# Kernel tuning notes

Hardware: AMD Instinct MI355X
Metric: run time of the kernel (lower is better)

Reference implementation:

```python
import jax, jax.numpy as jnp
import numpy as np

N_NODES = 50000
N_EDGES = 800000
IN_DIM, HID_DIM, OUT_DIM = 128, 128, 64


def _sage_conv(x, src, dst, W_l, W_r, b, num_nodes):
    # mean aggregation of source-node features onto destination nodes
    msg = x[src]  # [E, d] gather
    summed = jax.ops.segment_sum(msg, dst, num_segments=num_nodes)  # [N, d]
    deg = jax.ops.segment_sum(jnp.ones((src.shape[0],), dtype=x.dtype), dst,
                              num_segments=num_nodes)  # [N]
    agg = summed / jnp.maximum(deg, 1.0)[:, None]
    # SAGEConv: lin_l(agg) + lin_r(x); bias only on lin_l (PyG default)
    return agg @ W_l + b + x @ W_r


def setup_inputs() -> dict:
    key = jax.random.key(0)
    k = jax.random.split(key, 8)
    def glorot(kk, shape):
        lim = float(np.sqrt(6.0 / (shape[0] + shape[1])))
        return jax.random.uniform(kk, shape, jnp.float32, -lim, lim)
    return {
        "x": jax.random.normal(k[0], (N_NODES, IN_DIM), jnp.float32),
        "edge_index": jax.random.randint(k[1], (2, N_EDGES), 0, N_NODES, jnp.int64),
        "W1_l": glorot(k[2], (IN_DIM, HID_DIM)),
        "W1_r": glorot(k[3], (IN_DIM, HID_DIM)),
        "b1": jnp.zeros((HID_DIM,), jnp.float32),
        "W2_l": glorot(k[4], (HID_DIM, OUT_DIM)),
        "W2_r": glorot(k[5], (HID_DIM, OUT_DIM)),
        "b2": jnp.zeros((OUT_DIM,), jnp.float32),
    }


def reference(x, edge_index, W1_l, W1_r, b1, W2_l, W2_r, b2):
    src, dst = edge_index[0], edge_index[1]
    n = x.shape[0]
    h = _sage_conv(x, src, dst, W1_l, W1_r, b1, n)
    h = jax.nn.relu(h)
    # dropout is identity in eval mode
    out = _sage_conv(h, src, dst, W2_l, W2_r, b2, n)
    return out
```

## Files before the change

### kernel.cpp

```cpp
#include <hip/hip_runtime.h>
#include <hip/hip_bf16.h>


#define BLK 256

typedef __attribute__((ext_vector_type(8))) short short8;
typedef __attribute__((ext_vector_type(4))) float f32x4;

__device__ inline unsigned short f2bf(float f) {
    unsigned int u = __builtin_bit_cast(unsigned int, f);
    u += 0x7fffu + ((u >> 16) & 1u);
    return (unsigned short)(u >> 16);
}
__device__ inline float bf2f(unsigned short h) {
    return __builtin_bit_cast(float, ((unsigned int)h) << 16);
}


__global__ __launch_bounds__(BLK) void deg_count_kernel(const int* __restrict__ dst,
                                                        int E, int* __restrict__ deg) {
    int e = blockIdx.x * BLK + threadIdx.x;
    if (e < E) atomicAdd(&deg[dst[e]], 1);
}

__global__ __launch_bounds__(BLK) void partial_sum_kernel(const int* __restrict__ deg,
                                                          int n, int* __restrict__ partials) {
    __shared__ int s[BLK];
    int t = threadIdx.x;
    int idx = blockIdx.x * BLK + t;
    s[t] = (idx < n) ? deg[idx] : 0;
    __syncthreads();
    for (int o = BLK / 2; o > 0; o >>= 1) {
        if (t < o) s[t] += s[t + o];
        __syncthreads();
    }
    if (t == 0) partials[blockIdx.x] = s[0];
}

__global__ __launch_bounds__(BLK) void scan_partials_kernel(int* __restrict__ partials, int n) {
    __shared__ int s[BLK];
    int t = threadIdx.x;
    int v = (t < n) ? partials[t] : 0;
    s[t] = v;
    __syncthreads();
    int sum = v;
    for (int o = 1; o < BLK; o <<= 1) {
        int other = (t >= o) ? s[t - o] : 0;
        __syncthreads();
        sum += other;
        s[t] = sum;
        __syncthreads();
    }
    if (t < n) partials[t] = sum - v;
}

__global__ __launch_bounds__(BLK) void chunk_scan_kernel(const int* __restrict__ deg,
                                                         const int* __restrict__ partials,
                                                         int n, int* __restrict__ row_start) {
    __shared__ int s[BLK];
    int t = threadIdx.x;
    int idx = blockIdx.x * BLK + t;
    int v = (idx < n) ? deg[idx] : 0;
    s[t] = v;
    __syncthreads();
    int sum = v;
    for (int o = 1; o < BLK; o <<= 1) {
        int other = (t >= o) ? s[t - o] : 0;
        __syncthreads();
        sum += other;
        s[t] = sum;
        __syncthreads();
    }
    if (idx < n) row_start[idx] = (sum - v) + partials[blockIdx.x];
}

__global__ __launch_bounds__(BLK) void fill_kernel(const int* __restrict__ src,
                                                   const int* __restrict__ dst, int E,
                                                   const int* __restrict__ row_start,
                                                   int* __restrict__ cursor,
                                                   int* __restrict__ csr_src) {
    int e = blockIdx.x * BLK + threadIdx.x;
    if (e >= E) return;
    int d = dst[e];
    int pos = atomicAdd(&cursor[d], 1);
    atomicExch(&csr_src[row_start[d] + pos], src[e]);
}


__global__ __launch_bounds__(BLK) void f32_to_bf16_kernel(const float* __restrict__ in,
                                                          unsigned short* __restrict__ out,
                                                          int nquad) {
    int i = blockIdx.x * BLK + threadIdx.x;
    if (i >= nquad) return;
    float4 v = ((const float4*)in)[i];
    ushort4 o;
    o.x = f2bf(v.x); o.y = f2bf(v.y); o.z = f2bf(v.z); o.w = f2bf(v.w);
    ((ushort4*)out)[i] = o;
}

__global__ __launch_bounds__(BLK) void pack_all_w_kernel(const float* __restrict__ W1l,
                                                         const float* __restrict__ W1r,
                                                         const float* __restrict__ W2l,
                                                         const float* __restrict__ W2r,
                                                         unsigned short* __restrict__ P1l,
                                                         unsigned short* __restrict__ P1r,
                                                         unsigned short* __restrict__ P2l,
                                                         unsigned short* __restrict__ P2r) {
    int t = blockIdx.x * BLK + threadIdx.x;
    const float* W;
    unsigned short* P;
    int Ncol, local;
    if (t < 16384)      { W = W1l; P = P1l; Ncol = 128; local = t; }
    else if (t < 32768) { W = W1r; P = P1r; Ncol = 128; local = t - 16384; }
    else if (t < 40960) { W = W2l; P = P2l; Ncol = 64;  local = t - 32768; }
    else if (t < 49152) { W = W2r; P = P2r; Ncol = 64;  local = t - 40960; }
    else return;
    int j = local & 7;
    int lane = (local >> 3) & 63;
    int rest = local >> 9;
    int nt = Ncol >> 4;
    int n16 = rest % nt, kb = rest / nt;
    int k = kb * 32 + (lane >> 4) * 8 + j;
    int c = n16 * 16 + (lane & 15);
    P[local] = f2bf(W[(size_t)k * Ncol + c]);
}


__global__ __launch_bounds__(BLK) void agg_bf16_kernel(const unsigned short* __restrict__ feat,
                                                       const int* __restrict__ row_start,
                                                       const int* __restrict__ deg,
                                                       const int* __restrict__ csr_src,
                                                       unsigned short* __restrict__ out,
                                                       int n_nodes) {
    int gid = blockIdx.x * (BLK / 64) + (threadIdx.x >> 6);
    int lane = threadIdx.x & 63;
    if (gid >= n_nodes) return;
    int start = row_start[gid];
    int cnt = deg[gid];
    const unsigned int* fp = (const unsigned int*)feat;
    float ax[8], ay[8];
#pragma unroll
    for (int j = 0; j < 8; j++) { ax[j] = 0.f; ay[j] = 0.f; }

    for (int base = 0; base < cnt; base += 64) {
        int rem = cnt - base;
        int m = rem < 64 ? rem : 64;
        int idx = csr_src[start + base + (lane < m ? lane : m - 1)];
        int e = 0;
        for (; e + 8 <= m; e += 8) {
            unsigned int v[8];
#pragma unroll
            for (int j = 0; j < 8; j++) {
                int s = __shfl(idx, e + j);
                v[j] = fp[(size_t)s * 64 + lane];
            }
#pragma unroll
            for (int j = 0; j < 8; j++) {
                ax[j] += bf2f((unsigned short)v[j]);
                ay[j] += bf2f((unsigned short)(v[j] >> 16));
            }
        }
        for (; e < m; ++e) {
            int s = __shfl(idx, e);
            unsigned int v = fp[(size_t)s * 64 + lane];
            ax[0] += bf2f((unsigned short)v);
            ay[0] += bf2f((unsigned short)(v >> 16));
        }
    }
    float sx = ((ax[0] + ax[1]) + (ax[2] + ax[3])) + ((ax[4] + ax[5]) + (ax[6] + ax[7]));
    float sy = ((ay[0] + ay[1]) + (ay[2] + ay[3])) + ((ay[4] + ay[5]) + (ay[6] + ay[7]));
    float inv = 1.0f / fmaxf((float)cnt, 1.0f);
    unsigned int packed = (unsigned int)f2bf(sx * inv) | ((unsigned int)f2bf(sy * inv) << 16);
    ((unsigned int*)out)[(size_t)gid * 64 + lane] = packed;
}


template <int NCOL, bool RELU, bool OUT_BF16>
__global__ __launch_bounds__(BLK) void gemm_mfma_kernel(const unsigned short* __restrict__ A1,
                                                        const unsigned short* __restrict__ A2,
                                                        const unsigned short* __restrict__ Pl,
                                                        const unsigned short* __restrict__ Pr,
                                                        const float* __restrict__ bias,
                                                        void* __restrict__ outp, int M) {
    constexpr int NT = NCOL / 16;
    const int wave = threadIdx.x >> 6, lane = threadIdx.x & 63;
    const int r0 = blockIdx.x * 128 + wave * 32;
    const int arow = lane & 15, kgrp = lane >> 4;

    f32x4 acc[2][NT];
#pragma unroll
    for (int h = 0; h < 2; h++)
#pragma unroll
        for (int n = 0; n < NT; n++) acc[h][n] = (f32x4){0.f, 0.f, 0.f, 0.f};

    const int ra = min(r0 + arow, M - 1);
    const int rb = min(r0 + 16 + arow, M - 1);

#pragma unroll
    for (int mat = 0; mat < 2; ++mat) {
        const unsigned short* A = mat ? A2 : A1;
        const unsigned short* P = mat ? Pr : Pl;
        const unsigned short* Aa = A + (size_t)ra * 128 + kgrp * 8;
        const unsigned short* Ab = A + (size_t)rb * 128 + kgrp * 8;
#pragma unroll
        for (int kb = 0; kb < 4; ++kb) {
            short8 afa = *(const short8*)(Aa + kb * 32);
            short8 afb = *(const short8*)(Ab + kb * 32);
            const unsigned short* Pk = P + (size_t)kb * NT * 512 + lane * 8;
#pragma unroll
            for (int n = 0; n < NT; ++n) {
                short8 wf = *(const short8*)(Pk + n * 512);
                acc[0][n] = __builtin_amdgcn_mfma_f32_16x16x32_bf16(afa, wf, acc[0][n], 0, 0, 0);
                acc[1][n] = __builtin_amdgcn_mfma_f32_16x16x32_bf16(afb, wf, acc[1][n], 0, 0, 0);
            }
        }
    }

#pragma unroll
    for (int n = 0; n < NT; ++n) {
        int col = n * 16 + arow;
        float bv = bias[col];
#pragma unroll
        for (int h = 0; h < 2; ++h) {
#pragma unroll
            for (int i = 0; i < 4; ++i) {
                int row = r0 + h * 16 + kgrp * 4 + i;
                if (row < M) {
                    float v = acc[h][n][i] + bv;
                    if (RELU) v = fmaxf(v, 0.f);
                    if (OUT_BF16)
                        ((unsigned short*)outp)[(size_t)row * NCOL + col] = f2bf(v);
                    else
                        ((float*)outp)[(size_t)row * NCOL + col] = v;
                }
            }
        }
    }
}


extern "C" void kernel_launch(void* const* d_in, const int* in_sizes, int n_in,
                              void* d_out, int out_size, void* d_ws, size_t ws_size,
                              hipStream_t stream) {
    const float* x   = (const float*)d_in[0];
    const int*   ei  = (const int*)d_in[1];
    const float* W1l = (const float*)d_in[2];
    const float* W1r = (const float*)d_in[3];
    const float* b1  = (const float*)d_in[4];
    const float* W2l = (const float*)d_in[5];
    const float* W2r = (const float*)d_in[6];
    const float* b2  = (const float*)d_in[7];
    float* out = (float*)d_out;

    const int N = in_sizes[0] / 128;
    const int E = in_sizes[1] / 2;
    const int* src = ei;
    const int* dst = ei + E;

    char* ws = (char*)d_ws;
    size_t off = 0;
    auto carve = [&](size_t bytes) {
        void* p = ws + off;
        off += (bytes + 255) & ~(size_t)255;
        return p;
    };
    int* deg       = (int*)carve((size_t)2 * N * 4);
    int* cursor    = deg + N;
    int* row_start = (int*)carve((size_t)N * 4);
    int* partials  = (int*)carve(256 * 4);
    int* csr_src   = (int*)carve((size_t)E * 4);
    unsigned short* xb   = (unsigned short*)carve((size_t)N * 128 * 2);
    unsigned short* aggb = (unsigned short*)carve((size_t)N * 128 * 2);
    unsigned short* hb   = (unsigned short*)carve((size_t)N * 128 * 2);
    unsigned short* P1l  = (unsigned short*)carve(128 * 128 * 2);
    unsigned short* P1r  = (unsigned short*)carve(128 * 128 * 2);
    unsigned short* P2l  = (unsigned short*)carve(128 * 64 * 2);
    unsigned short* P2r  = (unsigned short*)carve(128 * 64 * 2);

    hipMemsetAsync(deg, 0, (size_t)2 * N * 4, stream);

    const int nquad = N * 128 / 4;
    f32_to_bf16_kernel<<<(nquad + BLK - 1) / BLK, BLK, 0, stream>>>(x, xb, nquad);
    pack_all_w_kernel<<<192, BLK, 0, stream>>>(W1l, W1r, W2l, W2r, P1l, P1r, P2l, P2r);

    const int nchunk = (N + BLK - 1) / BLK;
    deg_count_kernel<<<(E + BLK - 1) / BLK, BLK, 0, stream>>>(dst, E, deg);
    partial_sum_kernel<<<nchunk, BLK, 0, stream>>>(deg, N, partials);
    scan_partials_kernel<<<1, BLK, 0, stream>>>(partials, nchunk);
    chunk_scan_kernel<<<nchunk, BLK, 0, stream>>>(deg, partials, N, row_start);
    fill_kernel<<<(E + BLK - 1) / BLK, BLK, 0, stream>>>(src, dst, E, row_start, cursor, csr_src);

    const int aggGrid = (N + 3) / 4;
    const int gemmGrid = (N + 127) / 128;

    agg_bf16_kernel<<<aggGrid, BLK, 0, stream>>>(xb, row_start, deg, csr_src, aggb, N);
    gemm_mfma_kernel<128, true, true><<<gemmGrid, BLK, 0, stream>>>(aggb, xb, P1l, P1r, b1, hb, N);
    agg_bf16_kernel<<<aggGrid, BLK, 0, stream>>>(hb, row_start, deg, csr_src, aggb, N);
    gemm_mfma_kernel<64, false, false><<<gemmGrid, BLK, 0, stream>>>(aggb, hb, P2l, P2r, b2, out, N);
}
```

Measured before the change: 303.8 us.

## Slice features into XCD-local column blocks and partition CSR fill by destination range

Stores bf16 node features in 8 column slices of 16 features each, so each slice (N*32 bytes, about 1.6 MB) can stay resident in one XCD's L2. Aggregation blocks are interleaved by slice using blockIdx&7, and each wave gathers 8 edges at a time with 8 lanes per edge, then reduces across lanes with shuffles. The CSR fill is split by destination range per blockIdx octet with plain stores instead of atomicExch, aiming for L2-local atomics. The trade-off is 8x redundant reads of dst in the fill and of the CSR indices in the gather, more shuffle reductions, and strided A-operand loads in the GEMM. It also relies on blockIdx-to-XCD round-robin placement.

```diff
diff --git a/kernel.cpp b/kernel.cpp
--- a/kernel.cpp
+++ b/kernel.cpp
@@ -74,29 +74,46 @@
     if (idx < n) row_start[idx] = (sum - v) + partials[blockIdx.x];
 }
 
-__global__ __launch_bounds__(BLK) void fill_kernel(const int* __restrict__ src,
-                                                   const int* __restrict__ dst, int E,
-                                                   const int* __restrict__ row_start,
-                                                   int* __restrict__ cursor,
-                                                   int* __restrict__ csr_src) {
-    int e = blockIdx.x * BLK + threadIdx.x;
-    if (e >= E) return;
-    int d = dst[e];
-    int pos = atomicAdd(&cursor[d], 1);
-    atomicExch(&csr_src[row_start[d] + pos], src[e]);
-}
-
-
-__global__ __launch_bounds__(BLK) void f32_to_bf16_kernel(const float* __restrict__ in,
-                                                          unsigned short* __restrict__ out,
-                                                          int nquad) {
-    int i = blockIdx.x * BLK + threadIdx.x;
-    if (i >= nquad) return;
-    float4 v = ((const float4*)in)[i];
-    ushort4 o;
-    o.x = f2bf(v.x); o.y = f2bf(v.y); o.z = f2bf(v.z); o.w = f2bf(v.w);
-    ((ushort4*)out)[i] = o;
-}
+__global__ __launch_bounds__(BLK) void fill_xcd_kernel(const int* __restrict__ src,
+                                                       const int* __restrict__ dst, int E,
+                                                       const int* __restrict__ row_start,
+                                                       int* __restrict__ cursor,
+                                                       int* __restrict__ csr_src,
+                                                       int range, int CH) {
+    const int oct = blockIdx.x & 7;
+    const int chunk = blockIdx.x >> 3;
+    const int lo = oct * range, hi = lo + range;
+    int e0 = chunk * CH;
+    int e1 = min(E, e0 + CH);
+    for (int e = e0 + threadIdx.x; e < e1; e += BLK) {
+        int d = dst[e];
+        if (d >= lo && d < hi) {
+            int pos = atomicAdd(&cursor[d], 1);
+            csr_src[row_start[d] + pos] = src[e];
+        }
+    }
+}
+
+
+__global__ __launch_bounds__(BLK) void x_prep_kernel(const float* __restrict__ x,
+                                                     unsigned short* __restrict__ xT,
+                                                     int N) {
+    int node = blockIdx.x * BLK + threadIdx.x;
+    int slice = blockIdx.y;
+    if (node >= N) return;
+    const float4* xp = (const float4*)(x + (size_t)node * 128 + slice * 16);
+    unsigned int u[8];
+#pragma unroll
+    for (int q = 0; q < 4; ++q) {
+        float4 v = xp[q];
+        u[q * 2]     = (unsigned int)f2bf(v.x) | ((unsigned int)f2bf(v.y) << 16);
+        u[q * 2 + 1] = (unsigned int)f2bf(v.z) | ((unsigned int)f2bf(v.w) << 16);
+    }
+    uint4* o = (uint4*)(xT + ((size_t)slice * N + node) * 16);
+    o[0] = make_uint4(u[0], u[1], u[2], u[3]);
+    o[1] = make_uint4(u[4], u[5], u[6], u[7]);
+}
+
 
 __global__ __launch_bounds__(BLK) void pack_all_w_kernel(const float* __restrict__ W1l,
                                                          const float* __restrict__ W1r,
@@ -126,66 +143,61 @@
 }
 
 
-__global__ __launch_bounds__(BLK) void agg_bf16_kernel(const unsigned short* __restrict__ feat,
-                                                       const int* __restrict__ row_start,
-                                                       const int* __restrict__ deg,
-                                                       const int* __restrict__ csr_src,
-                                                       unsigned short* __restrict__ out,
-                                                       int n_nodes) {
-    int gid = blockIdx.x * (BLK / 64) + (threadIdx.x >> 6);
-    int lane = threadIdx.x & 63;
-    if (gid >= n_nodes) return;
-    int start = row_start[gid];
-    int cnt = deg[gid];
-    const unsigned int* fp = (const unsigned int*)feat;
-    float ax[8], ay[8];
-#pragma unroll
-    for (int j = 0; j < 8; j++) { ax[j] = 0.f; ay[j] = 0.f; }
-
-    for (int base = 0; base < cnt; base += 64) {
-        int rem = cnt - base;
-        int m = rem < 64 ? rem : 64;
-        int idx = csr_src[start + base + (lane < m ? lane : m - 1)];
-        int e = 0;
-        for (; e + 8 <= m; e += 8) {
-            unsigned int v[8];
-#pragma unroll
-            for (int j = 0; j < 8; j++) {
-                int s = __shfl(idx, e + j);
-                v[j] = fp[(size_t)s * 64 + lane];
-            }
-#pragma unroll
-            for (int j = 0; j < 8; j++) {
-                ax[j] += bf2f((unsigned short)v[j]);
-                ay[j] += bf2f((unsigned short)(v[j] >> 16));
-            }
-        }
-        for (; e < m; ++e) {
-            int s = __shfl(idx, e);
-            unsigned int v = fp[(size_t)s * 64 + lane];
-            ax[0] += bf2f((unsigned short)v);
-            ay[0] += bf2f((unsigned short)(v >> 16));
-        }
-    }
-    float sx = ((ax[0] + ax[1]) + (ax[2] + ax[3])) + ((ax[4] + ax[5]) + (ax[6] + ax[7]));
-    float sy = ((ay[0] + ay[1]) + (ay[2] + ay[3])) + ((ay[4] + ay[5]) + (ay[6] + ay[7]));
-    float inv = 1.0f / fmaxf((float)cnt, 1.0f);
-    unsigned int packed = (unsigned int)f2bf(sx * inv) | ((unsigned int)f2bf(sy * inv) << 16);
-    ((unsigned int*)out)[(size_t)gid * 64 + lane] = packed;
-}
-
-
-template <int NCOL, bool RELU, bool OUT_BF16>
-__global__ __launch_bounds__(BLK) void gemm_mfma_kernel(const unsigned short* __restrict__ A1,
-                                                        const unsigned short* __restrict__ A2,
-                                                        const unsigned short* __restrict__ Pl,
-                                                        const unsigned short* __restrict__ Pr,
-                                                        const float* __restrict__ bias,
-                                                        void* __restrict__ outp, int M) {
+__global__ __launch_bounds__(BLK) void agg_sliced_kernel(const unsigned short* __restrict__ fT,
+                                                         const int* __restrict__ row_start,
+                                                         const int* __restrict__ deg,
+                                                         const int* __restrict__ csr_src,
+                                                         unsigned short* __restrict__ aT,
+                                                         int N) {
+    const int wave = threadIdx.x >> 6, lane = threadIdx.x & 63;
+    const int slice = blockIdx.x & 7;
+    const int g = blockIdx.x >> 3;
+    const int cu = lane & 7;
+    const int es = lane >> 3;
+    const unsigned int* xs = (const unsigned int*)(fT + (size_t)slice * N * 16);
+    unsigned int* as = (unsigned int*)(aT + (size_t)slice * N * 16);
+
+    const int UN = 8;
+    int node0 = (g * 4 + wave) * UN;
+    for (int u = 0; u < UN; ++u) {
+        int node = node0 + u;
+        if (node >= N) return;
+        int start = row_start[node];
+        int cnt = deg[node];
+        float inv = 1.0f / fmaxf((float)cnt, 1.0f);
+        float s0 = 0.f, s1 = 0.f;
+        for (int e0 = 0; e0 < cnt; e0 += 8) {
+            int ee = e0 + es;
+            float w = (ee < cnt) ? inv : 0.0f;
+            int esel = (ee < cnt) ? ee : (cnt - 1);
+            int idx = csr_src[start + esel];
+            unsigned int v = xs[(size_t)idx * 8 + cu];
+            s0 = fmaf(bf2f((unsigned short)v), w, s0);
+            s1 = fmaf(bf2f((unsigned short)(v >> 16)), w, s1);
+        }
+#pragma unroll
+        for (int m = 8; m <= 32; m <<= 1) {
+            s0 += __shfl_xor(s0, m);
+            s1 += __shfl_xor(s1, m);
+        }
+        if (es == 0)
+            as[(size_t)node * 8 + cu] = (unsigned int)f2bf(s0) | ((unsigned int)f2bf(s1) << 16);
+    }
+}
+
+
+template <int NCOL, bool RELU, int OUTMODE>
+__global__ __launch_bounds__(BLK) void gemm_dual_T_kernel(const unsigned short* __restrict__ A1,
+                                                          const unsigned short* __restrict__ A2,
+                                                          const unsigned short* __restrict__ Pl,
+                                                          const unsigned short* __restrict__ Pr,
+                                                          const float* __restrict__ bias,
+                                                          void* __restrict__ outp, int M) {
     constexpr int NT = NCOL / 16;
     const int wave = threadIdx.x >> 6, lane = threadIdx.x & 63;
     const int r0 = blockIdx.x * 128 + wave * 32;
     const int arow = lane & 15, kgrp = lane >> 4;
+    const int kg2 = kgrp >> 1, off8 = (kgrp & 1) * 8;
 
     f32x4 acc[2][NT];
 #pragma unroll
@@ -195,17 +207,18 @@
 
     const int ra = min(r0 + arow, M - 1);
     const int rb = min(r0 + 16 + arow, M - 1);
+    const size_t sstride = (size_t)M * 16;
 
 #pragma unroll
     for (int mat = 0; mat < 2; ++mat) {
         const unsigned short* A = mat ? A2 : A1;
         const unsigned short* P = mat ? Pr : Pl;
-        const unsigned short* Aa = A + (size_t)ra * 128 + kgrp * 8;
-        const unsigned short* Ab = A + (size_t)rb * 128 + kgrp * 8;
+        const unsigned short* Aa = A + (size_t)kg2 * sstride + (size_t)ra * 16 + off8;
+        const unsigned short* Ab = A + (size_t)kg2 * sstride + (size_t)rb * 16 + off8;
 #pragma unroll
         for (int kb = 0; kb < 4; ++kb) {
-            short8 afa = *(const short8*)(Aa + kb * 32);
-            short8 afb = *(const short8*)(Ab + kb * 32);
+            short8 afa = *(const short8*)(Aa + (size_t)kb * 2 * sstride);
+            short8 afb = *(const short8*)(Ab + (size_t)kb * 2 * sstride);
             const unsigned short* Pk = P + (size_t)kb * NT * 512 + lane * 8;
 #pragma unroll
             for (int n = 0; n < NT; ++n) {
@@ -228,8 +241,9 @@
                 if (row < M) {
                     float v = acc[h][n][i] + bv;
                     if (RELU) v = fmaxf(v, 0.f);
-                    if (OUT_BF16)
-                        ((unsigned short*)outp)[(size_t)row * NCOL + col] = f2bf(v);
+                    if (OUTMODE == 1)
+                        ((unsigned short*)outp)[(size_t)n * M * 16 + (size_t)row * 16 + arow] =
+                            f2bf(v);
                     else
                         ((float*)outp)[(size_t)row * NCOL + col] = v;
                 }
@@ -269,9 +283,9 @@
     int* row_start = (int*)carve((size_t)N * 4);
     int* partials  = (int*)carve(256 * 4);
     int* csr_src   = (int*)carve((size_t)E * 4);
-    unsigned short* xb   = (unsigned short*)carve((size_t)N * 128 * 2);
-    unsigned short* aggb = (unsigned short*)carve((size_t)N * 128 * 2);
-    unsigned short* hb   = (unsigned short*)carve((size_t)N * 128 * 2);
+    unsigned short* xT   = (unsigned short*)carve((size_t)8 * N * 16 * 2);
+    unsigned short* hT   = (unsigned short*)carve((size_t)8 * N * 16 * 2);
+    unsigned short* aggT = (unsigned short*)carve((size_t)8 * N * 16 * 2);
     unsigned short* P1l  = (unsigned short*)carve(128 * 128 * 2);
     unsigned short* P1r  = (unsigned short*)carve(128 * 128 * 2);
     unsigned short* P2l  = (unsigned short*)carve(128 * 64 * 2);
@@ -279,8 +293,8 @@
 
     hipMemsetAsync(deg, 0, (size_t)2 * N * 4, stream);
 
-    const int nquad = N * 128 / 4;
-    f32_to_bf16_kernel<<<(nquad + BLK - 1) / BLK, BLK, 0, stream>>>(x, xb, nquad);
+    dim3 prepGrid((N + BLK - 1) / BLK, 8);
+    x_prep_kernel<<<prepGrid, BLK, 0, stream>>>(x, xT, N);
     pack_all_w_kernel<<<192, BLK, 0, stream>>>(W1l, W1r, W2l, W2r, P1l, P1r, P2l, P2r);
 
     const int nchunk = (N + BLK - 1) / BLK;
@@ -288,13 +302,18 @@
     partial_sum_kernel<<<nchunk, BLK, 0, stream>>>(deg, N, partials);
     scan_partials_kernel<<<1, BLK, 0, stream>>>(partials, nchunk);
     chunk_scan_kernel<<<nchunk, BLK, 0, stream>>>(deg, partials, N, row_start);
-    fill_kernel<<<(E + BLK - 1) / BLK, BLK, 0, stream>>>(src, dst, E, row_start, cursor, csr_src);
-
-    const int aggGrid = (N + 3) / 4;
+
+    const int range = (N + 7) / 8;
+    const int NCHUNKS = 512;
+    const int CH = (E + NCHUNKS - 1) / NCHUNKS;
+    fill_xcd_kernel<<<8 * NCHUNKS, BLK, 0, stream>>>(src, dst, E, row_start, cursor,
+                                                     csr_src, range, CH);
+
+    const int aggGrid = 8 * ((N + 31) / 32);
     const int gemmGrid = (N + 127) / 128;
 
-    agg_bf16_kernel<<<aggGrid, BLK, 0, stream>>>(xb, row_start, deg, csr_src, aggb, N);
-    gemm_mfma_kernel<128, true, true><<<gemmGrid, BLK, 0, stream>>>(aggb, xb, P1l, P1r, b1, hb, N);
-    agg_bf16_kernel<<<aggGrid, BLK, 0, stream>>>(hb, row_start, deg, csr_src, aggb, N);
-    gemm_mfma_kernel<64, false, false><<<gemmGrid, BLK, 0, stream>>>(aggb, hb, P2l, P2r, b2, out, N);
-}
+    agg_sliced_kernel<<<aggGrid, BLK, 0, stream>>>(xT, row_start, deg, csr_src, aggT, N);
+    gemm_dual_T_kernel<128, true, 1><<<gemmGrid, BLK, 0, stream>>>(aggT, xT, P1l, P1r, b1, hT, N);
+    agg_sliced_kernel<<<aggGrid, BLK, 0, stream>>>(hT, row_start, deg, csr_src, aggT, N);
+    gemm_dual_T_kernel<64, false, 0><<<gemmGrid, BLK, 0, stream>>>(aggT, hT, P2l, P2r, b2, out, N);
+}
```

New measurement: 393.8 us. 1.3x slower.

## Partition CSR fill by destination range per XCD and deepen aggregation gather batching

Applied to the files above, without the earlier changes.

The CSR fill kernel now launches 8 groups of blocks. Block index mod 8 selects a destination-node range, and each block scans one edge chunk, keeping only edges whose destination falls in its range. The intent is to keep atomics and scattered writes local to one XCD's L2, at the cost of every edge being read 8 times. The aggregation kernel now issues 16 gathered row loads per batch, using readlane instead of shuffles and masked weights instead of a scalar tail loop. It also folds the 1/deg scaling into an FMA with a single accumulator pair, trading extra work on padded lanes for more memory-level parallelism.

```diff
diff --git a/kernel.cpp b/kernel.cpp
--- a/kernel.cpp
+++ b/kernel.cpp
@@ -74,16 +74,24 @@
     if (idx < n) row_start[idx] = (sum - v) + partials[blockIdx.x];
 }
 
-__global__ __launch_bounds__(BLK) void fill_kernel(const int* __restrict__ src,
-                                                   const int* __restrict__ dst, int E,
-                                                   const int* __restrict__ row_start,
-                                                   int* __restrict__ cursor,
-                                                   int* __restrict__ csr_src) {
-    int e = blockIdx.x * BLK + threadIdx.x;
-    if (e >= E) return;
-    int d = dst[e];
-    int pos = atomicAdd(&cursor[d], 1);
-    atomicExch(&csr_src[row_start[d] + pos], src[e]);
+__global__ __launch_bounds__(BLK) void fill_xcd_kernel(const int* __restrict__ src,
+                                                       const int* __restrict__ dst, int E,
+                                                       const int* __restrict__ row_start,
+                                                       int* __restrict__ cursor,
+                                                       int* __restrict__ csr_src,
+                                                       int range, int CH) {
+    const int oct = blockIdx.x & 7;
+    const int chunk = blockIdx.x >> 3;
+    const int lo = oct * range, hi = lo + range;
+    int e0 = chunk * CH;
+    int e1 = min(E, e0 + CH);
+    for (int e = e0 + threadIdx.x; e < e1; e += BLK) {
+        int d = dst[e];
+        if (d >= lo && d < hi) {
+            int pos = atomicAdd(&cursor[d], 1);
+            csr_src[row_start[d] + pos] = src[e];
+        }
+    }
 }
 
 
@@ -126,57 +134,50 @@
 }
 
 
-__global__ __launch_bounds__(BLK) void agg_bf16_kernel(const unsigned short* __restrict__ feat,
-                                                       const int* __restrict__ row_start,
-                                                       const int* __restrict__ deg,
-                                                       const int* __restrict__ csr_src,
-                                                       unsigned short* __restrict__ out,
-                                                       int n_nodes) {
-    int gid = blockIdx.x * (BLK / 64) + (threadIdx.x >> 6);
-    int lane = threadIdx.x & 63;
-    if (gid >= n_nodes) return;
-    int start = row_start[gid];
-    int cnt = deg[gid];
+__global__ __launch_bounds__(BLK) void agg_mlp_kernel(const unsigned short* __restrict__ feat,
+                                                      const int* __restrict__ row_start,
+                                                      const int* __restrict__ deg,
+                                                      const int* __restrict__ csr_src,
+                                                      unsigned short* __restrict__ out,
+                                                      int N, int E) {
+    const int wave = threadIdx.x >> 6, lane = threadIdx.x & 63;
+    const int node = blockIdx.x * (BLK / 64) + wave;
+    if (node >= N) return;
+    const int start = __builtin_amdgcn_readfirstlane(row_start[node]);
+    int cnt = __builtin_amdgcn_readfirstlane(deg[node]);
+    cnt = min(cnt, E);
+    const float inv = 1.0f / fmaxf((float)cnt, 1.0f);
     const unsigned int* fp = (const unsigned int*)feat;
-    float ax[8], ay[8];
-#pragma unroll
-    for (int j = 0; j < 8; j++) { ax[j] = 0.f; ay[j] = 0.f; }
-
+
+    float a0 = 0.f, a1 = 0.f;
     for (int base = 0; base < cnt; base += 64) {
-        int rem = cnt - base;
-        int m = rem < 64 ? rem : 64;
-        int idx = csr_src[start + base + (lane < m ? lane : m - 1)];
-        int e = 0;
-        for (; e + 8 <= m; e += 8) {
-            unsigned int v[8];
-#pragma unroll
-            for (int j = 0; j < 8; j++) {
-                int s = __shfl(idx, e + j);
+        int m = cnt - base;
+        if (m > 64) m = 64;
+        int idxv = csr_src[start + base + (lane < m ? lane : m - 1)];
+        for (int e = 0; e < m; e += 16) {
+            unsigned int v[16];
+#pragma unroll
+            for (int j = 0; j < 16; j++) {
+                int ee = e + j;
+                int sl = ee < m ? ee : m - 1;
+                int s = __builtin_amdgcn_readlane(idxv, sl);
                 v[j] = fp[(size_t)s * 64 + lane];
             }
 #pragma unroll
-            for (int j = 0; j < 8; j++) {
-                ax[j] += bf2f((unsigned short)v[j]);
-                ay[j] += bf2f((unsigned short)(v[j] >> 16));
+            for (int j = 0; j < 16; j++) {
+                float w = (e + j < m) ? inv : 0.0f;
+                a0 = fmaf(bf2f((unsigned short)v[j]), w, a0);
+                a1 = fmaf(bf2f((unsigned short)(v[j] >> 16)), w, a1);
             }
         }
-        for (; e < m; ++e) {
-            int s = __shfl(idx, e);
-            unsigned int v = fp[(size_t)s * 64 + lane];
-            ax[0] += bf2f((unsigned short)v);
-            ay[0] += bf2f((unsigned short)(v >> 16));
-        }
-    }
-    float sx = ((ax[0] + ax[1]) + (ax[2] + ax[3])) + ((ax[4] + ax[5]) + (ax[6] + ax[7]));
-    float sy = ((ay[0] + ay[1]) + (ay[2] + ay[3])) + ((ay[4] + ay[5]) + (ay[6] + ay[7]));
-    float inv = 1.0f / fmaxf((float)cnt, 1.0f);
-    unsigned int packed = (unsigned int)f2bf(sx * inv) | ((unsigned int)f2bf(sy * inv) << 16);
-    ((unsigned int*)out)[(size_t)gid * 64 + lane] = packed;
+    }
+    ((unsigned int*)out)[(size_t)node * 64 + lane] =
+        (unsigned int)f2bf(a0) | ((unsigned int)f2bf(a1) << 16);
 }
 
 
 template <int NCOL, bool RELU, bool OUT_BF16>
-__global__ __launch_bounds__(BLK) void gemm_mfma_kernel(const unsigned short* __restrict__ A1,
+__global__ __launch_bounds__(BLK) void gemm_dual_kernel(const unsigned short* __restrict__ A1,
                                                         const unsigned short* __restrict__ A2,
                                                         const unsigned short* __restrict__ Pl,
                                                         const unsigned short* __restrict__ Pr,
@@ -288,13 +289,18 @@
     partial_sum_kernel<<<nchunk, BLK, 0, stream>>>(deg, N, partials);
     scan_partials_kernel<<<1, BLK, 0, stream>>>(partials, nchunk);
     chunk_scan_kernel<<<nchunk, BLK, 0, stream>>>(deg, partials, N, row_start);
-    fill_kernel<<<(E + BLK - 1) / BLK, BLK, 0, stream>>>(src, dst, E, row_start, cursor, csr_src);
+
+    const int range = (N + 7) / 8;
+    const int NCHUNKS = 512;
+    const int CH = (E + NCHUNKS - 1) / NCHUNKS;
+    fill_xcd_kernel<<<8 * NCHUNKS, BLK, 0, stream>>>(src, dst, E, row_start, cursor,
+                                                     csr_src, range, CH);
 
     const int aggGrid = (N + 3) / 4;
     const int gemmGrid = (N + 127) / 128;
 
-    agg_bf16_kernel<<<aggGrid, BLK, 0, stream>>>(xb, row_start, deg, csr_src, aggb, N);
-    gemm_mfma_kernel<128, true, true><<<gemmGrid, BLK, 0, stream>>>(aggb, xb, P1l, P1r, b1, hb, N);
-    agg_bf16_kernel<<<aggGrid, BLK, 0, stream>>>(hb, row_start, deg, csr_src, aggb, N);
-    gemm_mfma_kernel<64, false, false><<<gemmGrid, BLK, 0, stream>>>(aggb, hb, P2l, P2r, b2, out, N);
-}
+    agg_mlp_kernel<<<aggGrid, BLK, 0, stream>>>(xb, row_start, deg, csr_src, aggb, N, E);
+    gemm_dual_kernel<128, true, true><<<gemmGrid, BLK, 0, stream>>>(aggb, xb, P1l, P1r, b1, hb, N);
+    agg_mlp_kernel<<<aggGrid, BLK, 0, stream>>>(hb, row_start, deg, csr_src, aggb, N, E);
+    gemm_dual_kernel<64, false, false><<<gemmGrid, BLK, 0, stream>>>(aggb, hb, P2l, P2r, b2, out, N);
+}
```

Measured after the change: 265.5 us. 12.6% less time.
